# Kernel tuning notes

Hardware: AMD Instinct MI355X
Metric: run time of the kernel (lower is better)

Reference implementation:

```python
import jax, jax.numpy as jnp
import numpy as np

B, S, D, H, HD = 2, 2048, 1024, 16, 64
DFF = 4 * D
EPS = 1e-6


def _rms(x, w):
    return w * (x * jax.lax.rsqrt(jnp.mean(x * x, axis=-1, keepdims=True) + EPS))


def _rope(x, rope):
    # x: [B, H, S, HD], rope: [S, HD, 2]
    cos = rope[..., 0][None, None]
    sin = rope[..., 1][None, None]
    xr = x.reshape(*x.shape[:-1], -1, 2)
    rot = jnp.stack([-xr[..., 1], xr[..., 0]], axis=-1).reshape(x.shape)
    return x * cos + rot * sin


def setup_inputs() -> dict:
    key = jax.random.key(0)
    ks = jax.random.split(key, 10)
    w = lambda k, shape: jax.random.normal(k, shape, jnp.float32) * 0.02
    return {
        "hidden_states": jax.random.normal(ks[0], (B, S, D), jnp.float32),
        "timestep": jax.random.normal(ks[1], (B, D), jnp.float32),
        "rope_pos_embed": jax.random.normal(ks[2], (S, HD, 2), jnp.float32),
        "adaln_w": w(ks[3], (6 * D, D)),
        "adaln_b": jnp.zeros((6 * D,), jnp.float32),
        "wq": w(ks[4], (D, D)),
        "wk": w(ks[5], (D, D)),
        "wv": w(ks[6], (D, D)),
        "wo": w(ks[7], (D, D)),
        "q_norm_w": jnp.ones((D,), jnp.float32),
        "k_norm_w": jnp.ones((D,), jnp.float32),
        "norm3_w": jnp.ones((D,), jnp.float32),
        "fc1_w": w(ks[8], (DFF, D)),
        "fc1_b": jnp.zeros((DFF,), jnp.float32),
        "fc2_w": w(ks[9], (D, DFF)),
        "fc2_b": jnp.zeros((D,), jnp.float32),
    }


def reference(hidden_states, timestep, rope_pos_embed, adaln_w, adaln_b,
              wq, wk, wv, wo, q_norm_w, k_norm_w, norm3_w,
              fc1_w, fc1_b, fc2_w, fc2_b):
    x = hidden_states  # [B, S, D]
    # AdaLayerNorm: emb = Linear(SiLU(timestep)) -> 6 modulation chunks, broadcast over seq
    emb = jax.nn.silu(timestep) @ adaln_w.T + adaln_b  # [B, 6D]
    sh_msa, sc_msa, g_msa, sh_mlp, sc_mlp, g_mlp = jnp.split(emb[:, None, :], 6, axis=-1)
    mu = jnp.mean(x, axis=-1, keepdims=True)
    var = jnp.mean((x - mu) ** 2, axis=-1, keepdims=True)
    ln = (x - mu) * jax.lax.rsqrt(var + EPS)
    xm = ln * (1.0 + sc_msa) + sh_msa  # modulated input to attention

    # Attention: projections + RMSNorm over inner_dim + RoPE + SDPA
    q = _rms(xm @ wq.T, q_norm_w)
    k = _rms(xm @ wk.T, k_norm_w)
    v = xm @ wv.T
    q = q.reshape(B, S, H, HD).transpose(0, 2, 1, 3)
    k = k.reshape(B, S, H, HD).transpose(0, 2, 1, 3)
    v = v.reshape(B, S, H, HD).transpose(0, 2, 1, 3)
    q = _rope(q, rope_pos_embed)
    k = _rope(k, rope_pos_embed)
    scores = jnp.einsum('bhqd,bhkd->bhqk', q, k) * (HD ** -0.5)
    attn = jax.nn.softmax(scores, axis=-1)
    o = jnp.einsum('bhqk,bhkd->bhqd', attn, v)
    o = o.transpose(0, 2, 1, 3).reshape(B, S, H * HD) @ wo.T

    h = x + g_msa * o  # gated residual

    # MLP branch with AdaLN scale/shift on RMSNorm output
    n3 = _rms(h, norm3_w)
    nm = n3 * (1.0 + sc_mlp) + sh_mlp
    ff = jax.nn.gelu(nm @ fc1_w.T + fc1_b, approximate=True) @ fc2_w.T + fc2_b
    return h + g_mlp * ff
```

## Files before the change

### kernel.cpp

```cpp
#include <hip/hip_runtime.h>
#include <cstdint>
#include <cstddef>

typedef unsigned short ushort_t;
typedef __attribute__((ext_vector_type(8))) short s8v;
typedef __attribute__((ext_vector_type(4))) short s4v;
typedef __attribute__((ext_vector_type(4))) float f4v;

#define MFMA16(a, b, c) __builtin_amdgcn_mfma_f32_16x16x32_bf16(a, b, c, 0, 0, 0)

__device__ __forceinline__ ushort_t f2bf(float f) {
  union { float f; unsigned u; } a; a.f = f;
  return (ushort_t)((a.u + 0x7fffu + ((a.u >> 16) & 1u)) >> 16);
}
__device__ __forceinline__ float bf2f(ushort_t h) {
  union { unsigned u; float f; } a; a.u = ((unsigned)h) << 16; return a.f;
}
__device__ __forceinline__ unsigned fbits(float f) {
  union { float f; unsigned u; } a; a.f = f; return a.u;
}

__device__ __forceinline__ void gload16(const void* g, void* l) {
  __builtin_amdgcn_global_load_lds(
      (__attribute__((address_space(1))) void*)(uintptr_t)g,
      (__attribute__((address_space(3))) void*)(unsigned)(uintptr_t)l,
      16, 0, 0);
}

__launch_bounds__(256)
__global__ void convert_w(const float* __restrict__ wq, const float* __restrict__ wk,
                          const float* __restrict__ wv, const float* __restrict__ wo,
                          const float* __restrict__ f1, const float* __restrict__ f2,
                          ushort_t* __restrict__ dqkv, ushort_t* __restrict__ dwo,
                          ushort_t* __restrict__ df1, ushort_t* __restrict__ df2)
{
  const int blk = blockIdx.x;
  const float* src; ushort_t* dst; int off;
  if      (blk < 1024) { src = wq; dst = dqkv;            off = blk; }
  else if (blk < 2048) { src = wk; dst = dqkv + 1048576;  off = blk - 1024; }
  else if (blk < 3072) { src = wv; dst = dqkv + 2097152;  off = blk - 2048; }
  else if (blk < 4096) { src = wo; dst = dwo;             off = blk - 3072; }
  else if (blk < 8192) { src = f1; dst = df1;             off = blk - 4096; }
  else                 { src = f2; dst = df2;             off = blk - 8192; }
  const int idx = off * 1024 + threadIdx.x * 4;
  float4 v = *(const float4*)(src + idx);
  s4v o;
  o[0] = (short)f2bf(v.x); o[1] = (short)f2bf(v.y);
  o[2] = (short)f2bf(v.z); o[3] = (short)f2bf(v.w);
  *(s4v*)(dst + idx) = o;
}

__launch_bounds__(256)
__global__ void adaln(const float* __restrict__ ts, const float* __restrict__ w,
                      const float* __restrict__ bias, float* __restrict__ emb)
{
  const int j = blockIdx.x * 4 + (threadIdx.x >> 6);
  const int lane = threadIdx.x & 63;
  const float* wr = w + (size_t)j * 1024;
  float s0 = 0.f, s1 = 0.f;
  for (int i = lane; i < 1024; i += 64) {
    const float wv = wr[i];
    const float t0 = ts[i], t1 = ts[1024 + i];
    const float e0 = __builtin_amdgcn_exp2f(-1.4426950409f * t0);
    const float e1 = __builtin_amdgcn_exp2f(-1.4426950409f * t1);
    s0 += wv * t0 * __builtin_amdgcn_rcpf(1.f + e0);
    s1 += wv * t1 * __builtin_amdgcn_rcpf(1.f + e1);
  }
  #pragma unroll
  for (int m = 32; m; m >>= 1) { s0 += __shfl_down(s0, m); s1 += __shfl_down(s1, m); }
  if (!lane) { emb[j] = s0 + bias[j]; emb[6144 + j] = s1 + bias[j]; }
}

__launch_bounds__(256)
__global__ void ln_mod(const float* __restrict__ x, const float* __restrict__ emb,
                       ushort_t* __restrict__ xm)
{
  const int row = blockIdx.x, b = row >> 11, tid = threadIdx.x;
  const float* xr = x + (size_t)row * 1024;
  const int c = tid * 4;
  float4 v = *(const float4*)(xr + c);
  float s  = v.x + v.y + v.z + v.w;
  float s2 = v.x*v.x + v.y*v.y + v.z*v.z + v.w*v.w;
  #pragma unroll
  for (int m = 32; m; m >>= 1) { s += __shfl_down(s, m); s2 += __shfl_down(s2, m); }
  __shared__ float red[8];
  const int wave = tid >> 6, lane = tid & 63;
  if (!lane) { red[wave] = s; red[4 + wave] = s2; }
  __syncthreads();
  const float mu = (red[0] + red[1] + red[2] + red[3]) * (1.f / 1024.f);
  const float ms = (red[4] + red[5] + red[6] + red[7]) * (1.f / 1024.f);
  const float rstd = rsqrtf(ms - mu * mu + 1e-6f);
  const float* sh = emb + b * 6144;
  const float* sc = emb + b * 6144 + 1024;
  float4 shv = *(const float4*)(sh + c);
  float4 scv = *(const float4*)(sc + c);
  s4v ov;
  ov[0] = (short)f2bf((v.x - mu) * rstd * (1.f + scv.x) + shv.x);
  ov[1] = (short)f2bf((v.y - mu) * rstd * (1.f + scv.y) + shv.y);
  ov[2] = (short)f2bf((v.z - mu) * rstd * (1.f + scv.z) + shv.z);
  ov[3] = (short)f2bf((v.w - mu) * rstd * (1.f + scv.w) + shv.w);
  *(s4v*)(xm + (size_t)row * 1024 + c) = ov;
}

template<int EPI, int TN>
__launch_bounds__(256, 4)
__global__ void gemm_bt(const ushort_t* __restrict__ A, const ushort_t* __restrict__ Bw,
                        int K, int N,
                        ushort_t* __restrict__ outb, float* __restrict__ outf,
                        const float* __restrict__ bias, const float* __restrict__ resid,
                        const float* __restrict__ emb, int gate_off)
{
  constexpr int JN = TN / 32;
  constexpr int BUFB = TN * 32;
  __shared__ ushort_t As0[128 * 32], As1[128 * 32];
  __shared__ ushort_t Bs0[BUFB],    Bs1[BUFB];
  const int tid = threadIdx.x;
  const int wave = tid >> 6, lane = tid & 63;
  const int quad = lane >> 4, r = lane & 15;

  const int nwg = gridDim.x * gridDim.y;
  int wg = blockIdx.y * gridDim.x + blockIdx.x;
  wg = (wg & 7) * (nwg >> 3) + (wg >> 3);
  const int bx = wg % gridDim.x, by = wg / gridDim.x;
  const int m0 = by * 128, n0 = bx * TN;
  const int wm = (wave >> 1) * 64, wn = (wave & 1) * (TN / 2);

  const int srow = wave * 16 + (lane >> 2);
  const int scol = (lane & 3) * 8;
  const ushort_t* ag = A  + (size_t)(m0 + srow) * K + scol;
  const ushort_t* bg = Bw + (size_t)(n0 + srow) * K + scol;
  const size_t rowK64 = (size_t)64 * K;

  f4v acc[4][JN] = {};

  auto stage = [&](ushort_t* as, ushort_t* bs) {
    gload16(ag,          as + wave * 512);
    gload16(ag + rowK64, as + wave * 512 + 2048);
    gload16(bg,          bs + wave * 512);
    if (TN == 128) gload16(bg + rowK64, bs + wave * 512 + 2048);
    ag += 32; bg += 32;
  };
  auto compute = [&](const ushort_t* ab, const ushort_t* bb) {
    s8v af[4], bf[JN];
    #pragma unroll
    for (int i = 0; i < 4; i++)
      af[i] = *(const s8v*)(ab + (wm + i * 16 + r) * 32 + quad * 8);
    #pragma unroll
    for (int j = 0; j < JN; j++)
      bf[j] = *(const s8v*)(bb + (wn + j * 16 + r) * 32 + quad * 8);
    #pragma unroll
    for (int i = 0; i < 4; i++)
      #pragma unroll
      for (int j = 0; j < JN; j++)
        acc[i][j] = MFMA16(af[i], bf[j], acc[i][j]);
  };

  stage(As0, Bs0);
  __syncthreads();
  const int R = (K >> 6) - 1;
  for (int it = 0; it < R; it++) {
    stage(As1, Bs1);
    compute(As0, Bs0);
    __syncthreads();
    stage(As0, Bs0);
    compute(As1, Bs1);
    __syncthreads();
  }
  stage(As1, Bs1);
  compute(As0, Bs0);
  __syncthreads();
  compute(As1, Bs1);

  const int bblk = m0 >> 11;
  float bj[JN], gj[JN];
  #pragma unroll
  for (int j = 0; j < JN; j++) {
    const int col = n0 + wn + j * 16 + r;
    bj[j] = (EPI == 2 || EPI == 3) ? bias[col] : 0.f;
    gj[j] = (EPI == 1 || EPI == 3) ? emb[bblk * 6144 + gate_off + col] : 0.f;
  }
  #pragma unroll
  for (int i = 0; i < 4; i++) {
    #pragma unroll
    for (int rr = 0; rr < 4; rr++) {
      const int row = m0 + wm + i * 16 + quad * 4 + rr;
      const size_t rbase = (size_t)row * N + n0 + wn;
      #pragma unroll
      for (int j = 0; j < JN; j++) {
        float v = acc[i][j][rr];
        const size_t idx = rbase + j * 16 + r;
        if (EPI == 0) {
          outb[idx] = f2bf(v);
        } else if (EPI == 1) {
          outf[idx] = resid[idx] + gj[j] * v;
        } else if (EPI == 2) {
          v += bj[j];
          const float t = fmaf(v * v, 0.1029436f, 2.3022083f);
          const float e = __builtin_amdgcn_exp2f(-v * t);
          outb[idx] = f2bf(v * __builtin_amdgcn_rcpf(1.f + e));
        } else {
          outf[idx] = resid[idx] + gj[j] * (v + bj[j]);
        }
      }
    }
  }
}

__launch_bounds__(256)
__global__ void qkv_post(const ushort_t* __restrict__ qkv, const float* __restrict__ rope,
                         const float* __restrict__ qw, const float* __restrict__ kw,
                         ushort_t* __restrict__ q_r, ushort_t* __restrict__ k_r,
                         ushort_t* __restrict__ v_r)
{
  const int row = blockIdx.x, b = row >> 11, s = row & 2047, tid = threadIdx.x;
  const ushort_t* base = qkv + (size_t)row * 3072;
  const int c = tid * 4;
  s4v qv = *(const s4v*)(base + c);
  s4v kv = *(const s4v*)(base + 1024 + c);
  s4v vv = *(const s4v*)(base + 2048 + c);
  float qf[4], kf[4]; float sq = 0.f, sk = 0.f;
  #pragma unroll
  for (int i = 0; i < 4; i++) {
    qf[i] = bf2f((ushort_t)qv[i]); kf[i] = bf2f((ushort_t)kv[i]);
    sq += qf[i] * qf[i]; sk += kf[i] * kf[i];
  }
  #pragma unroll
  for (int m = 32; m; m >>= 1) { sq += __shfl_down(sq, m); sk += __shfl_down(sk, m); }
  __shared__ float red[8];
  const int wave = tid >> 6, lane = tid & 63;
  if (!lane) { red[wave] = sq; red[4 + wave] = sk; }
  __syncthreads();
  const float rq = rsqrtf((red[0]+red[1]+red[2]+red[3]) * (1.f/1024.f) + 1e-6f)
                   * 0.18033688011112042f;
  const float rk = rsqrtf((red[4]+red[5]+red[6]+red[7]) * (1.f/1024.f) + 1e-6f);

  const int h = c >> 6, d = c & 63;
  const float* rp = rope + ((size_t)s * 64 + d) * 2;
  float4 r01 = *(const float4*)(rp);
  float4 r23 = *(const float4*)(rp + 4);
  const float q0 = qf[0]*rq*qw[c], q1 = qf[1]*rq*qw[c+1];
  const float q2 = qf[2]*rq*qw[c+2], q3 = qf[3]*rq*qw[c+3];
  const float k0 = kf[0]*rk*kw[c], k1 = kf[1]*rk*kw[c+1];
  const float k2 = kf[2]*rk*kw[c+2], k3 = kf[3]*rk*kw[c+3];
  s4v qo, ko;
  qo[0] = (short)f2bf(q0 * r01.x - q1 * r01.y);
  qo[1] = (short)f2bf(q1 * r01.z + q0 * r01.w);
  qo[2] = (short)f2bf(q2 * r23.x - q3 * r23.y);
  qo[3] = (short)f2bf(q3 * r23.z + q2 * r23.w);
  ko[0] = (short)f2bf(k0 * r01.x - k1 * r01.y);
  ko[1] = (short)f2bf(k1 * r01.z + k0 * r01.w);
  ko[2] = (short)f2bf(k2 * r23.x - k3 * r23.y);
  ko[3] = (short)f2bf(k3 * r23.z + k2 * r23.w);
  const size_t rowbase = ((size_t)(b * 16 + h) * 2048 + s) * 64;
  const int d_s = (((d >> 3) ^ (s & 7)) << 3) | (d & 7);
  *(s4v*)(q_r + rowbase + d) = qo;
  *(s4v*)(k_r + rowbase + d_s) = ko;
  *(s4v*)(v_r + rowbase + d) = vv;
}

__launch_bounds__(256)
__global__ void vtrans(const ushort_t* __restrict__ v_r, ushort_t* __restrict__ v_t)
{
  const int bh = blockIdx.x >> 5, st = blockIdx.x & 31;
  const int s0 = st * 64;
  __shared__ ushort_t tile[64 * 72];
  const int tid = threadIdx.x;
  #pragma unroll
  for (int rep = 0; rep < 2; rep++) {
    const int idx = rep * 256 + tid;
    const int sr = idx >> 3, dc = (idx & 7) << 3;
    s8v val = *(const s8v*)(v_r + ((size_t)bh * 2048 + s0 + sr) * 64 + dc);
    *(s8v*)(tile + sr * 72 + dc) = val;
  }
  __syncthreads();
  #pragma unroll
  for (int rep = 0; rep < 2; rep++) {
    const int idx = rep * 256 + tid;
    const int d = idx >> 3;
    const int scs = (((idx & 7) ^ (d & 7)) << 3);
    s8v val;
    const int sc = (idx & 7) << 3;
    #pragma unroll
    for (int j = 0; j < 8; j++) val[j] = (short)tile[(sc + j) * 72 + d];
    *(s8v*)(v_t + ((size_t)bh * 64 + d) * 2048 + s0 + scs) = val;
  }
}

__launch_bounds__(256, 4)
__global__ void flash(const ushort_t* __restrict__ q_r, const ushort_t* __restrict__ k_r,
                      const ushort_t* __restrict__ v_t, ushort_t* __restrict__ attn)
{
  __shared__ ushort_t Ksh[2][64 * 64];
  __shared__ ushort_t Vsh[2][64 * 64];
  __shared__ ushort_t Psh[4][16 * 64];
  const int bh = blockIdx.x >> 5, qb = blockIdx.x & 31;
  const int tid = threadIdx.x, wave = tid >> 6, lane = tid & 63;
  const int quad = lane >> 4, r = lane & 15;
  const int rx = r & 7;
  const int q0 = qb * 64 + wave * 16;
  const size_t bhS = (size_t)bh * 2048;

  s8v aq0 = *(const s8v*)(q_r + (bhS + q0 + r) * 64 + quad * 8);
  s8v aq1 = *(const s8v*)(q_r + (bhS + q0 + r) * 64 + 32 + quad * 8);

  f4v o[4] = {};
  float mi = -1e30f, li = 0.f;

  const ushort_t* kg = k_r + (bhS + wave * 16 + (lane >> 3)) * 64 + (lane & 7) * 8;
  const ushort_t* vg = v_t + ((size_t)bh * 64 + wave * 16 + (lane >> 3)) * 2048
                       + (lane & 7) * 8;
  const int klo = wave * 1024 + lane * 8;
  const int vlo = wave * 1024 + lane * 8;
  ushort_t* pw = &Psh[wave][0];

  auto stage = [&](ushort_t* kbuf, ushort_t* vbuf, int kb) {
    #pragma unroll
    for (int c = 0; c < 2; c++) {
      gload16(kg + (size_t)(kb + c * 8) * 64, kbuf + klo + c * 512);
      gload16(vg + kb + (size_t)(c * 8) * 2048, vbuf + vlo + c * 512);
    }
  };

  auto step = [&](const ushort_t* Kc, const ushort_t* Vc) {
    f4v st[4];
    __builtin_amdgcn_s_setprio(1);
    #pragma unroll
    for (int t = 0; t < 4; t++) {
      const ushort_t* krow = Kc + (t * 16 + r) * 64;
      s8v k0 = *(const s8v*)(krow + ((quad ^ rx) << 3));
      s8v k1 = *(const s8v*)(krow + (((4 + quad) ^ rx) << 3));
      f4v z = {};
      z = MFMA16(k0, aq0, z);
      z = MFMA16(k1, aq1, z);
      st[t] = z;
    }
    __builtin_amdgcn_s_setprio(0);

    float m4[4];
    #pragma unroll
    for (int t = 0; t < 4; t++)
      m4[t] = fmaxf(fmaxf(st[t][0], st[t][1]), fmaxf(st[t][2], st[t][3]));
    float mloc = fmaxf(fmaxf(m4[0], m4[1]), fmaxf(m4[2], m4[3]));
    mloc = fmaxf(mloc, __shfl_xor(mloc, 16));
    mloc = fmaxf(mloc, __shfl_xor(mloc, 32));

    const bool grow = !__all(mloc - mi <= 8.f);
    const float mref = grow ? fmaxf(mi, mloc) : mi;

    float p[4][4];
    uint2 pk[4];
    #pragma unroll
    for (int t = 0; t < 4; t++) {
      #pragma unroll
      for (int rr = 0; rr < 4; rr++)
        p[t][rr] = __builtin_amdgcn_exp2f(st[t][rr] - mref);
      const unsigned u0 = fbits(p[t][0]) + 0x8000u;
      const unsigned u1 = fbits(p[t][1]) + 0x8000u;
      const unsigned u2 = fbits(p[t][2]) + 0x8000u;
      const unsigned u3 = fbits(p[t][3]) + 0x8000u;
      pk[t].x = __builtin_amdgcn_perm(u1, u0, 0x07060302u);
      pk[t].y = __builtin_amdgcn_perm(u3, u2, 0x07060302u);
    }

    #pragma unroll
    for (int t = 0; t < 4; t++) {
      const int cw = t * 2 + (quad >> 1);
      const int sc = cw ^ rx;
      *(uint2*)(pw + r * 64 + (sc << 3) + (quad & 1) * 4) = pk[t];
    }

    if (grow) {
      const float al = __builtin_amdgcn_exp2f(mi - mref);
      float alo[4];
      #pragma unroll
      for (int rr = 0; rr < 4; rr++) alo[rr] = __shfl(al, quad * 4 + rr);
      #pragma unroll
      for (int nt = 0; nt < 4; nt++)
        #pragma unroll
        for (int rr = 0; rr < 4; rr++) o[nt][rr] *= alo[rr];
      li *= al;
      mi = mref;
    }

    float s4r[4];
    #pragma unroll
    for (int t = 0; t < 4; t++)
      s4r[t] = (p[t][0] + p[t][1]) + (p[t][2] + p[t][3]);
    float ls = (s4r[0] + s4r[1]) + (s4r[2] + s4r[3]);
    ls += __shfl_xor(ls, 16);
    ls += __shfl_xor(ls, 32);
    li += ls;

    asm volatile("s_waitcnt lgkmcnt(0)" ::: "memory");

    __builtin_amdgcn_s_setprio(1);
    #pragma unroll
    for (int kc = 0; kc < 2; kc++) {
      const int c = kc * 4 + quad;
      const int sc = c ^ rx;
      s8v ap = *(const s8v*)(pw + r * 64 + (sc << 3));
      #pragma unroll
      for (int nt = 0; nt < 4; nt++) {
        s8v bv = *(const s8v*)(Vc + (nt * 16 + r) * 64 + (sc << 3));
        o[nt] = MFMA16(ap, bv, o[nt]);
      }
    }
    __builtin_amdgcn_s_setprio(0);
  };

  stage(Ksh[0], Vsh[0], 0);
  __syncthreads();

  #pragma unroll 1
  for (int kb = 0; kb < 2048; kb += 128) {
    stage(Ksh[1], Vsh[1], kb + 64);
    step(Ksh[0], Vsh[0]);
    __syncthreads();
    if (kb + 128 < 2048) stage(Ksh[0], Vsh[0], kb + 128);
    step(Ksh[1], Vsh[1]);
    __syncthreads();
  }

  const int h = bh & 15, b = bh >> 4;
  const float linv = 1.f / li;
  #pragma unroll
  for (int rr = 0; rr < 4; rr++) {
    const float inv = __shfl(linv, quad * 4 + rr);
    const size_t orow = ((size_t)(b * 2048 + q0 + quad * 4 + rr)) * 1024 + h * 64;
    #pragma unroll
    for (int nt = 0; nt < 4; nt++)
      attn[orow + nt * 16 + r] = f2bf(o[nt][rr] * inv);
  }
}

__launch_bounds__(256)
__global__ void rms3_mod(const float* __restrict__ h, const float* __restrict__ emb,
                         const float* __restrict__ w3, ushort_t* __restrict__ nm)
{
  const int row = blockIdx.x, b = row >> 11, tid = threadIdx.x;
  const float* hr = h + (size_t)row * 1024;
  const int c = tid * 4;
  float4 v = *(const float4*)(hr + c);
  float s2 = v.x*v.x + v.y*v.y + v.z*v.z + v.w*v.w;
  #pragma unroll
  for (int m = 32; m; m >>= 1) s2 += __shfl_down(s2, m);
  __shared__ float red[4];
  const int wave = tid >> 6, lane = tid & 63;
  if (!lane) red[wave] = s2;
  __syncthreads();
  const float rms = rsqrtf((red[0] + red[1] + red[2] + red[3]) * (1.f / 1024.f) + 1e-6f);
  const float* sh = emb + b * 6144 + 3072;
  const float* sc = emb + b * 6144 + 4096;
  float4 shv = *(const float4*)(sh + c);
  float4 scv = *(const float4*)(sc + c);
  float4 wv  = *(const float4*)(w3 + c);
  s4v ov;
  ov[0] = (short)f2bf(v.x * rms * wv.x * (1.f + scv.x) + shv.x);
  ov[1] = (short)f2bf(v.y * rms * wv.y * (1.f + scv.y) + shv.y);
  ov[2] = (short)f2bf(v.z * rms * wv.z * (1.f + scv.z) + shv.z);
  ov[3] = (short)f2bf(v.w * rms * wv.w * (1.f + scv.w) + shv.w);
  *(s4v*)(nm + (size_t)row * 1024 + c) = ov;
}

extern "C" void kernel_launch(void* const* d_in, const int* in_sizes, int n_in,
                              void* d_out, int out_size, void* d_ws, size_t ws_size,
                              hipStream_t stream)
{
  const float* x    = (const float*)d_in[0];
  const float* ts   = (const float*)d_in[1];
  const float* rope = (const float*)d_in[2];
  const float* adw  = (const float*)d_in[3];
  const float* adb  = (const float*)d_in[4];
  const float* wq   = (const float*)d_in[5];
  const float* wk   = (const float*)d_in[6];
  const float* wv   = (const float*)d_in[7];
  const float* wo   = (const float*)d_in[8];
  const float* qnw  = (const float*)d_in[9];
  const float* knw  = (const float*)d_in[10];
  const float* n3w  = (const float*)d_in[11];
  const float* f1w  = (const float*)d_in[12];
  const float* f1b  = (const float*)d_in[13];
  const float* f2w  = (const float*)d_in[14];
  const float* f2b  = (const float*)d_in[15];

  char* ws = (char*)d_ws;
  ushort_t* WQKV = (ushort_t*)(ws + 0);
  ushort_t* WO   = (ushort_t*)(ws + 6291456);
  ushort_t* F1   = (ushort_t*)(ws + 8388608);
  ushort_t* F2   = (ushort_t*)(ws + 16777216);
  float*    EMB  = (float*)   (ws + 25165824);
  float*    H    = (float*)   (ws + 25214976);
  ushort_t* XM   = (ushort_t*)(ws + 41992192);
  ushort_t* QKV  = (ushort_t*)(ws + 50380800);
  ushort_t* QR   = (ushort_t*)(ws + 75546624);
  ushort_t* KR   = (ushort_t*)(ws + 83935232);
  ushort_t* VR   = (ushort_t*)(ws + 92323840);
  ushort_t* VT   = (ushort_t*)(ws + 100712448);
  ushort_t* ATTN = XM;
  ushort_t* NM   = QKV;
  ushort_t* FF1  = QR;

  convert_w<<<12288, 256, 0, stream>>>(wq, wk, wv, wo, f1w, f2w, WQKV, WO, F1, F2);
  adaln<<<1536, 256, 0, stream>>>(ts, adw, adb, EMB);
  ln_mod<<<4096, 256, 0, stream>>>(x, EMB, XM);
  gemm_bt<0, 128><<<dim3(24, 32), 256, 0, stream>>>(XM, WQKV, 1024, 3072,
      QKV, nullptr, nullptr, nullptr, nullptr, 0);
  qkv_post<<<4096, 256, 0, stream>>>(QKV, rope, qnw, knw, QR, KR, VR);
  vtrans<<<1024, 256, 0, stream>>>(VR, VT);
  flash<<<1024, 256, 0, stream>>>(QR, KR, VT, ATTN);
  gemm_bt<1, 64><<<dim3(16, 32), 256, 0, stream>>>(ATTN, WO, 1024, 1024,
      nullptr, H, nullptr, x, EMB, 2048);
  rms3_mod<<<4096, 256, 0, stream>>>(H, EMB, n3w, NM);
  gemm_bt<2, 128><<<dim3(32, 32), 256, 0, stream>>>(NM, F1, 1024, 4096,
      FF1, nullptr, f1b, nullptr, nullptr, 0);
  gemm_bt<3, 64><<<dim3(16, 32), 256, 0, stream>>>(FF1, F2, 4096, 1024,
      nullptr, (float*)d_out, f2b, H, EMB, 5120);
}
```

Measured before the change: 394.6 us.

## Add 256x256 eight-wave GEMM kernel for QKV and FC1 projections

Introduces a new GEMM kernel with 256x256 output tiles, 512 threads, double-buffered LDS filled through direct global-to-LDS loads, XOR-swizzled layout, an XCD-aware block remap and raised wave priority around the MFMA bursts. It replaces the 128-tile gemm_bt for the QKV projection and the FC1+GELU projection, aiming for more data reuse per tile and better overlap of loads with matrix math. The larger tiles produce fewer workgroups (192 and 256) on a GPU with 256 CUs, which risks lower occupancy and wave-quantization loss, and the tile shape requires K and N to be multiples of 256 and 64.

```diff
diff --git a/kernel.cpp b/kernel.cpp
--- a/kernel.cpp
+++ b/kernel.cpp
@@ -200,6 +200,113 @@
           outb[idx] = f2bf(v * __builtin_amdgcn_rcpf(1.f + e));
         } else {
           outf[idx] = resid[idx] + gj[j] * (v + bj[j]);
+        }
+      }
+    }
+  }
+}
+
+template<int EPI>
+__launch_bounds__(512, 1)
+__global__ void gemm8p(const ushort_t* __restrict__ A, const ushort_t* __restrict__ Bw,
+                       int K, int N, ushort_t* __restrict__ outb,
+                       const float* __restrict__ bias)
+{
+  __shared__ ushort_t Ash[2][4][256 * 16];
+  __shared__ ushort_t Bsh[2][4][256 * 16];
+  const int tid = threadIdx.x;
+  const int wid = tid >> 6, lane = tid & 63;
+  const int quad = lane >> 4, r = lane & 15;
+
+  const int nwg = gridDim.x * gridDim.y;
+  int wg = blockIdx.y * gridDim.x + blockIdx.x;
+  wg = (wg & 7) * (nwg >> 3) + (wg >> 3);
+  const int bx = wg % gridDim.x, by = wg / gridDim.x;
+  const int m0 = by * 256, n0 = bx * 256;
+  const int wm = (wid >> 2) * 128;
+  const int wn = (wid & 3) * 64;
+
+  const int srow = lane >> 1;
+  const int hsrc = (lane & 1) ^ ((lane >> 3) & 1);
+  const ushort_t* ag = A  + (size_t)(m0 + wid * 32 + srow) * K + hsrc * 8;
+  const ushort_t* bg = Bw + (size_t)(n0 + wid * 32 + srow) * K + hsrc * 8;
+  const int ldst = wid * 512 + lane * 8;
+
+  const int hq = ((quad & 1) ^ ((r >> 2) & 1)) * 8;
+  const int cq = (quad >> 1) * 4096;
+
+  f4v acc[8][4] = {};
+
+  auto ST = [&](int bufi, int kt, int kk) {
+    const size_t ko = (size_t)kt * 64 + kk * 32;
+    ushort_t* Ad = &Ash[bufi][2 * kk][ldst];
+    ushort_t* Bd = &Bsh[bufi][2 * kk][ldst];
+    gload16(ag + ko,      Ad);
+    gload16(bg + ko,      Bd);
+    gload16(ag + ko + 16, Ad + 4096);
+    gload16(bg + ko + 16, Bd + 4096);
+  };
+
+  auto PH = [&](const ushort_t* Ac, const ushort_t* Bc,
+                int stgbuf, int stgkt, int stgkk, bool dostg, bool vm4) {
+    if (vm4) asm volatile("s_waitcnt vmcnt(4)" ::: "memory");
+    else     asm volatile("s_waitcnt vmcnt(0)" ::: "memory");
+    __builtin_amdgcn_s_barrier();
+    const ushort_t* Acc = Ac + cq;
+    const ushort_t* Bcc = Bc + cq;
+    s8v af[8], bf[4];
+    #pragma unroll
+    for (int i = 0; i < 8; i++)
+      af[i] = *(const s8v*)(Acc + (wm + i * 16 + r) * 16 + hq);
+    #pragma unroll
+    for (int j = 0; j < 4; j++)
+      bf[j] = *(const s8v*)(Bcc + (wn + j * 16 + r) * 16 + hq);
+    if (dostg) ST(stgbuf, stgkt, stgkk);
+    asm volatile("s_waitcnt lgkmcnt(0)" ::: "memory");
+    __builtin_amdgcn_sched_barrier(0);
+    __builtin_amdgcn_s_setprio(1);
+    #pragma unroll
+    for (int i = 0; i < 8; i++)
+      #pragma unroll
+      for (int j = 0; j < 4; j++)
+        acc[i][j] = MFMA16(af[i], bf[j], acc[i][j]);
+    __builtin_amdgcn_s_setprio(0);
+  };
+
+  ST(0, 0, 0);
+  ST(0, 0, 1);
+
+  const int NT = K >> 6;
+  #pragma unroll 1
+  for (int t = 0; t < NT; t += 2) {
+    PH(&Ash[0][0][0], &Bsh[0][0][0], 1, t + 1, 0, true, true);
+    PH(&Ash[0][2][0], &Bsh[0][2][0], 1, t + 1, 1, true, true);
+    const bool s2 = (t + 2) < NT;
+    PH(&Ash[1][0][0], &Bsh[1][0][0], 0, t + 2, 0, s2, true);
+    PH(&Ash[1][2][0], &Bsh[1][2][0], 0, t + 2, 1, s2, s2);
+  }
+
+  float bj[4];
+  #pragma unroll
+  for (int j = 0; j < 4; j++)
+    bj[j] = (EPI == 2) ? bias[n0 + wn + j * 16 + r] : 0.f;
+  #pragma unroll
+  for (int i = 0; i < 8; i++) {
+    #pragma unroll
+    for (int rr = 0; rr < 4; rr++) {
+      const int row = m0 + wm + i * 16 + quad * 4 + rr;
+      const size_t rbase = (size_t)row * N + n0 + wn;
+      #pragma unroll
+      for (int j = 0; j < 4; j++) {
+        float v = acc[i][j][rr];
+        const size_t idx = rbase + j * 16 + r;
+        if (EPI == 0) {
+          outb[idx] = f2bf(v);
+        } else {
+          v += bj[j];
+          const float tt = fmaf(v * v, 0.1029436f, 2.3022083f);
+          const float e = __builtin_amdgcn_exp2f(-v * tt);
+          outb[idx] = f2bf(v * __builtin_amdgcn_rcpf(1.f + e));
         }
       }
     }
@@ -503,16 +610,14 @@
   convert_w<<<12288, 256, 0, stream>>>(wq, wk, wv, wo, f1w, f2w, WQKV, WO, F1, F2);
   adaln<<<1536, 256, 0, stream>>>(ts, adw, adb, EMB);
   ln_mod<<<4096, 256, 0, stream>>>(x, EMB, XM);
-  gemm_bt<0, 128><<<dim3(24, 32), 256, 0, stream>>>(XM, WQKV, 1024, 3072,
-      QKV, nullptr, nullptr, nullptr, nullptr, 0);
+  gemm8p<0><<<dim3(12, 16), 512, 0, stream>>>(XM, WQKV, 1024, 3072, QKV, nullptr);
   qkv_post<<<4096, 256, 0, stream>>>(QKV, rope, qnw, knw, QR, KR, VR);
   vtrans<<<1024, 256, 0, stream>>>(VR, VT);
   flash<<<1024, 256, 0, stream>>>(QR, KR, VT, ATTN);
   gemm_bt<1, 64><<<dim3(16, 32), 256, 0, stream>>>(ATTN, WO, 1024, 1024,
       nullptr, H, nullptr, x, EMB, 2048);
   rms3_mod<<<4096, 256, 0, stream>>>(H, EMB, n3w, NM);
-  gemm_bt<2, 128><<<dim3(32, 32), 256, 0, stream>>>(NM, F1, 1024, 4096,
-      FF1, nullptr, f1b, nullptr, nullptr, 0);
+  gemm8p<2><<<dim3(16, 16), 512, 0, stream>>>(NM, F1, 1024, 4096, FF1, f1b);
   gemm_bt<3, 64><<<dim3(16, 32), 256, 0, stream>>>(FF1, F2, 4096, 1024,
       nullptr, (float*)d_out, f2b, H, EMB, 5120);
 }
```

Result: no change. 387.1 us (-1.9%).
